# Kernel optimization log

Measured on AMD Instinct MI355X. Metric: run time of the kernel, lower is better.

Reference implementation:

```python
import jax, jax.numpy as jnp
import numpy as np
from jax.scipy.special import betainc

B, N, F_IN, D = 128, 50, 64, 64
E = N * (N - 1)          # fully-connected directed graph (no self loops)
S = N - 1                # number of ablation submodels
BN_ = B * N
EPS = 1e-5
NEG = jnp.float32(-1e9)
ALPHA = 0.05
SLOPE = 0.2              # LeakyReLU negative slope in GAT attention


def _build_graph():
    # edges grouped by target p: (c, p) for all c != p
    dst = np.repeat(np.arange(N), N - 1)
    src = np.concatenate([np.concatenate([np.arange(p), np.arange(p + 1, N)]) for p in range(N)])
    return src.astype(np.int64), dst.astype(np.int64)


def setup_inputs():
    key = jax.random.key(0)
    k = jax.random.split(key, 16)
    src, dst = _build_graph()
    edge_index = jnp.asarray(np.stack([src, dst]))
    offs = np.repeat(np.arange(B) * N, E)
    # batched edge list (get_batch_edge_index) + self loops appended (GraphLayer add_self_loops)
    src_b = jnp.asarray(np.concatenate([np.tile(src, B) + offs, np.arange(BN_)]))
    dst_b = jnp.asarray(np.concatenate([np.tile(dst, B) + offs, np.arange(BN_)]))
    # submodel s (s>=1) removes, for each target p, its (s-1)-th incoming neighbor (edge order)
    masks = np.ones((S + 1, E), dtype=bool)
    rem = np.empty((S, N), dtype=np.int64)
    for s in range(S):
        for p in range(N):
            e = p * (N - 1) + s
            masks[s + 1, e] = False
            rem[s, p] = e
    g = lambda kk, sh, sc: jax.random.normal(kk, sh, jnp.float32) * sc
    return dict(
        data=g(k[0], (B, N, F_IN), 1.0),
        labels=g(k[1], (B, N), 1.0),
        edge_index=edge_index,
        src_b=src_b, dst_b=dst_b,
        submodel_masks=jnp.asarray(masks),
        removed_edge_id=jnp.asarray(rem),
        emb=g(k[2], (N, D), 0.2),
        W_lin=g(k[3], (F_IN, D), F_IN ** -0.5),
        att_i=g(k[4], (D,), D ** -0.5), att_j=g(k[5], (D,), D ** -0.5),
        att_em_i=g(k[6], (D,), D ** -0.5), att_em_j=g(k[7], (D,), D ** -0.5),
        gat_bias=jnp.zeros((D,), jnp.float32),
        bn1_g=jnp.ones((D,), jnp.float32), bn1_b=jnp.zeros((D,), jnp.float32),
        bn1_rm=jnp.zeros((D,), jnp.float32), bn1_rv=jnp.ones((D,), jnp.float32),
        bn2_g=jnp.ones((D,), jnp.float32), bn2_b=jnp.zeros((D,), jnp.float32),
        bn2_rm=jnp.zeros((D,), jnp.float32), bn2_rv=jnp.ones((D,), jnp.float32),
        out_w=g(k[8], (D, 1), D ** -0.5), out_b=jnp.zeros((1,), jnp.float32),
    )


def reference(data, labels, edge_index, src_b, dst_b, submodel_masks, removed_edge_id,
              emb, W_lin, att_i, att_j, att_em_i, att_em_j, gat_bias,
              bn1_g, bn1_b, bn1_rm, bn1_rv, bn2_g, bn2_b, bn2_rm, bn2_rv, out_w, out_b):
    x_flat = data.reshape(BN_, F_IN)
    emb_nodes = jnp.tile(emb, (B, 1))            # all_embeddings = embedding.repeat(batch,1)

    def gnn(mask_E, train):
        # GDN-style GraphLayer: lin -> per-edge attn on (x||emb) keys -> segment softmax over dst
        emask = jnp.concatenate([jnp.tile(mask_E, B), jnp.ones(BN_, bool)])  # self loops kept
        h = x_flat @ W_lin                                  # [BN_, D]
        s_i = h @ att_i + emb_nodes @ att_em_i              # per-node dst score (key_i . att_i_cat)
        s_j = h @ att_j + emb_nodes @ att_em_j              # per-node src score
        logits = jax.nn.leaky_relu(s_i[dst_b] + s_j[src_b], SLOPE)
        logits = jnp.where(emask, logits, NEG)
        m = jax.ops.segment_max(logits, dst_b, num_segments=BN_)
        p = jnp.where(emask, jnp.exp(logits - m[dst_b]), 0.0)
        denom = jax.ops.segment_sum(p, dst_b, num_segments=BN_)
        alpha = p / denom[dst_b]
        out = jax.ops.segment_sum(alpha[:, None] * h[src_b], dst_b, num_segments=BN_) + gat_bias
        if train:
            mu, var = out.mean(0), out.var(0)               # BatchNorm1d training stats
        else:
            mu, var = bn1_rm, bn1_rv                        # eval mode (causal-edge search)
        return jax.nn.relu((out - mu) / jnp.sqrt(var + EPS) * bn1_g + bn1_b)

    def head(gcn, train):
        x3 = gcn.reshape(B, N, D) * emb[None]               # mul by node embedding
        if train:
            mu, var = x3.mean((0, 1)), x3.var((0, 1))       # BN over (B, N) per channel D
        else:
            mu, var = bn2_rm, bn2_rv
        xn = jax.nn.relu((x3 - mu) / jnp.sqrt(var + EPS) * bn2_g + bn2_b)
        return (xn @ out_w + out_b)[..., 0]                 # OutLayer (layer_num=1) -> [B,N]

    # --- causal ANOVA pruning: S+1 submodel forwards in eval mode (torch.no_grad) ---
    def body(_, mask_E):
        return None, head(gnn(mask_E, False), False)
    _, preds = jax.lax.scan(body, None, submodel_masks)     # [S+1, B, N]
    R = labels[None] - preds
    a, b = R[1:], R[0]                                      # ablated / full-graph residuals
    ma, mb = a.mean(1), b.mean(0)                           # [S,N], [N]
    grand = 0.5 * (ma + mb)
    ssb = B * ((ma - grand) ** 2 + (mb - grand) ** 2)       # between-group SS (df1=1)
    ssw = ((a - ma[:, None, :]) ** 2).sum(1) + ((b - mb) ** 2).sum(0)
    df2 = jnp.float32(2 * B - 2)
    fstat = ssb / (ssw / df2)
    pval = betainc(df2 / 2, 0.5, df2 / (df2 + fstat))       # sf of F(1, 2B-2) == f_oneway p
    prune = (pval > ALPHA).reshape(-1)                      # [S*N] == [E]
    keep = jnp.ones(E, bool).at[removed_edge_id.reshape(-1)].set(~prune)
    keep = jax.lax.stop_gradient(keep)

    # --- final forward on causally-learned graph (training-mode BN, dropout = identity) ---
    return head(gnn(keep, True), True)                      # [B, N]
```

## Files before the change

kernel.cpp:

```cpp
#include <hip/hip_runtime.h>
#include <math.h>

#define B_   128
#define N_   50
#define FIN  64
#define D_   64
#define BN   6400
#define EPSF 1e-5f
#define FCRIT 3.8783305f

__device__ __forceinline__ float wsum(float v){
#pragma unroll
  for(int o=32;o>0;o>>=1) v += __shfl_xor(v,o);
  return v;
}
__device__ __forceinline__ float wmax(float v){
#pragma unroll
  for(int o=32;o>0;o>>=1) v = fmaxf(v,__shfl_xor(v,o));
  return v;
}
__device__ __forceinline__ float leaky(float x){ return x >= 0.f ? x : 0.2f*x; }

__global__ __launch_bounds__(256) void k1_lin(
    const float* __restrict__ x, const float* __restrict__ W,
    const float* __restrict__ emb,
    const float* __restrict__ att_i, const float* __restrict__ att_j,
    const float* __restrict__ att_em_i, const float* __restrict__ att_em_j,
    const float* __restrict__ bn1_g, const float* __restrict__ bn1_b,
    const float* __restrict__ bn1_rm, const float* __restrict__ bn1_rv,
    const float* __restrict__ bn2_g, const float* __restrict__ bn2_b,
    const float* __restrict__ bn2_rm, const float* __restrict__ bn2_rv,
    const float* __restrict__ gat_bias, const float* __restrict__ out_w,
    float* __restrict__ h, float* __restrict__ s_i, float* __restrict__ s_j,
    float2* __restrict__ acc, float* __restrict__ statz ,
    float4* __restrict__ hc4, float* __restrict__ hci2g){
  __shared__ float wl[FIN*D_];
  __shared__ float xl[8*FIN];
  int tid = threadIdx.x;
  const float4* W4 = (const float4*)W;
  float4* wl4 = (float4*)wl;
  for(int i=tid;i<FIN*D_/4;i+=256) wl4[i] = W4[i];
  int r0 = blockIdx.x*8;
  { const float4* x4 = (const float4*)(x + (size_t)r0*FIN);
    float4* xl4 = (float4*)xl;
    for(int i=tid;i<8*FIN/4;i+=256) xl4[i] = x4[i]; }
  __syncthreads();
  int w = tid>>6, d = tid&63;
  float acc0 = 0.f, acc1 = 0.f;
#pragma unroll
  for(int k=0;k<FIN;k++){
    float wv = wl[k*D_+d];
    acc0 = fmaf(xl[(w*2+0)*FIN+k], wv, acc0);
    acc1 = fmaf(xl[(w*2+1)*FIN+k], wv, acc1);
  }
  float ai = att_i[d], aj = att_j[d], aei = att_em_i[d], aej = att_em_j[d];
#pragma unroll
  for(int j=0;j<2;j++){
    int r = r0 + w*2 + j;
    float a_ = j ? acc1 : acc0;
    h[(size_t)r*D_+d] = a_;
    int n = r % N_;
    float e = emb[n*D_+d];
    float si = wsum(a_*ai + e*aei);
    float sj = wsum(a_*aj + e*aej);
    if(d==0){ s_i[r]=si; s_j[r]=sj; }
  }
  if(blockIdx.x==0){
    for(int i=tid;i<N_*N_;i+=256) acc[i] = make_float2(0.f,0.f);
    for(int i=tid;i<2048;i+=256)  statz[i] = 0.f;
    if(tid < 64){
      float i1g = bn1_g[tid]/sqrtf(bn1_rv[tid]+EPSF);
      float i2g = bn2_g[tid]/sqrtf(bn2_rv[tid]+EPSF);
      float C1 = i1g*gat_bias[tid] + bn1_b[tid] - bn1_rm[tid]*i1g;
      float C2 = bn2_b[tid] - bn2_rm[tid]*i2g;
      hc4[tid] = make_float4(i1g, C1, C2, out_w[tid]);
      hci2g[tid] = i2g;
    }
  }
}

__global__ __launch_bounds__(512) void k2_preds(
    const float* __restrict__ h, const float* __restrict__ s_i,
    const float* __restrict__ s_j, const float* __restrict__ labels,
    const float* __restrict__ emb, const float* __restrict__ out_b,
    const float4* __restrict__ hc4, const float* __restrict__ hci2g,
    float2* __restrict__ acc){
  __shared__ float hT[64*53];
  __shared__ float el[8*64];
  __shared__ float2 wc[8*64];
  int b = blockIdx.y, tid = threadIdx.x;
  const float* hb = h + (size_t)b*N_*D_;
  for(int i=tid;i<N_*D_;i+=512) hT[(i&63)*53 + (i>>6)] = hb[i];
  __syncthreads();
  int w = tid>>6, lane = tid&63;
  int p = blockIdx.x*8 + w;
  if(p >= N_) return;
  float sip = s_i[b*N_+p];
  float L = -3.0e38f;
  if(lane < N_) L = leaky(sip + s_j[b*N_+lane]);
  float M = wmax(L);
  float e = (lane < N_) ? expf(L - M) : 0.f;
  float Dden = wsum(e);
  el[w*64+lane] = e;
  float S = 0.f;
  const float* hTd = &hT[lane*53];
  const float* elw = &el[w*64];
#pragma unroll 10
  for(int q=0;q<N_;q++) S = fmaf(elw[q], hTd[q], S);
  wc[w*64+lane] = make_float2(S, emb[p*D_+lane]*hci2g[lane]);
  float er = 0.f; int r = 0;
  if(lane >= 1 && lane < N_){
    int s = lane-1; r = s + (s>=p ? 1 : 0); er = el[w*64+r];
  }
  float beta = 1.f/(Dden - er);
  float alpha = er*beta;
  float acc_ = out_b[0];
  const float2* wcw = &wc[w*64];
#pragma unroll 8
  for(int d=0;d<64;d++){
    float4 hc = hc4[d];
    float2 se = wcw[d];
    float hrd = hT[d*53 + r];
    float o  = fmaf(-alpha, hrd, se.x*beta);
    float g  = fmaxf(fmaf(hc.x, o, hc.y), 0.f);
    float xn = fmaxf(fmaf(g, se.y, hc.z), 0.f);
    acc_ = fmaf(xn, hc.w, acc_);
  }
  if(lane < N_){
    float resid = labels[b*N_+p] - acc_;
    atomicAdd(&acc[p*N_+lane].x, resid);
    atomicAdd(&acc[p*N_+lane].y, resid*resid);
  }
}

__global__ __launch_bounds__(512) void k4a_out(
    const float* __restrict__ h, const float* __restrict__ s_i,
    const float* __restrict__ s_j, const float2* __restrict__ acc,
    const float* __restrict__ gat_bias,
    float* __restrict__ out_raw, float* __restrict__ stats1){
  __shared__ float hT[64*53];
  __shared__ float al[8*64];
  __shared__ int   keepL[8*64];
  __shared__ float2 red[8][64];
  int b = blockIdx.y, tid = threadIdx.x;
  const float* hb = h + (size_t)b*N_*D_;
  for(int i=tid;i<N_*D_;i+=512) hT[(i&63)*53 + (i>>6)] = hb[i];
  __syncthreads();
  int w = tid>>6, lane = tid&63;
  int p = blockIdx.x*8 + w;
  bool act = (p < N_);
  float o = 0.f;
  if(act){
    int kb = 1;
    if(lane < N_-1){
      float2 A2 = acc[p*N_ + lane + 1];
      float2 B2 = acc[p*N_];
      float ma = A2.x*(1.f/B_), mb = B2.x*(1.f/B_);
      float ssw = (A2.y - (float)B_*ma*ma) + (B2.y - (float)B_*mb*mb);
      float dmb = ma - mb;
      float f = (64.f*dmb*dmb) / (ssw*(1.f/254.f));
      kb = (f < FCRIT) ? 0 : 1;
    }
    keepL[w*64+lane] = kb;
    float sip = s_i[b*N_+p];
    float L = -3.0e38f; bool allowed = false;
    if(lane < N_){
      float Lr = leaky(sip + s_j[b*N_+lane]);
      if(lane == p) allowed = true;
      else { int idx = (lane < p) ? lane : lane-1; allowed = keepL[w*64+idx] != 0; }
      L = allowed ? Lr : -1.0e9f;
    }
    float M = wmax(L);
    float e = allowed ? expf(L - M) : 0.f;
    float Dn = wsum(e);
    al[w*64+lane] = e;
    float invD = 1.f/Dn;
    float s = 0.f;
    const float* hTd = &hT[lane*53];
    const float* alw = &al[w*64];
#pragma unroll 10
    for(int q=0;q<N_;q++) s = fmaf(alw[q], hTd[q], s);
    o = s*invD + gat_bias[lane];
    out_raw[((size_t)b*N_+p)*D_ + lane] = o;
  }
  red[w][lane] = act ? make_float2(o, o*o) : make_float2(0.f, 0.f);
  __syncthreads();
  if(w==0){
    float s1=0.f, s2=0.f;
#pragma unroll
    for(int k=0;k<8;k++){ float2 v = red[k][lane]; s1+=v.x; s2+=v.y; }
    int slot = b & 7;
    atomicAdd(&stats1[slot*128 + lane],      s1);
    atomicAdd(&stats1[slot*128 + 64 + lane], s2);
  }
}

__global__ __launch_bounds__(256) void k4b_stats(
    const float* __restrict__ out_raw, const float* __restrict__ emb,
    const float* __restrict__ bn1_g, const float* __restrict__ bn1_b,
    const float* __restrict__ stats1, float* __restrict__ stats2){
  __shared__ float2 red[4][64];
  int tid = threadIdx.x, w = tid>>6, lane = tid&63;
  float t1=0.f, t2=0.f;
#pragma unroll
  for(int k=0;k<8;k++){ t1 += stats1[k*128+lane]; t2 += stats1[k*128+64+lane]; }
  float mu1  = t1*(1.f/BN);
  float var1 = t2*(1.f/BN) - mu1*mu1;
  float A = bn1_g[lane]/sqrtf(var1+EPSF);
  float C = bn1_b[lane] - mu1*A;
  int r0 = blockIdx.x*64;
  float s1=0.f, s2=0.f;
  for(int i=w;i<64;i+=4){
    int r = r0+i;
    float o = out_raw[(size_t)r*D_ + lane];
    float g = fmaxf(fmaf(A,o,C), 0.f);
    float x3 = g*emb[(r%N_)*D_ + lane];
    s1 += x3; s2 = fmaf(x3,x3,s2);
  }
  red[w][lane] = make_float2(s1,s2);
  __syncthreads();
  if(w==0){
    float2 a=red[0][lane], b=red[1][lane], c=red[2][lane], d=red[3][lane];
    int slot = blockIdx.x & 7;
    atomicAdd(&stats2[slot*128 + lane],      a.x+b.x+c.x+d.x);
    atomicAdd(&stats2[slot*128 + 64 + lane], a.y+b.y+c.y+d.y);
  }
}

__global__ __launch_bounds__(256) void k4c_final(
    const float* __restrict__ out_raw, const float* __restrict__ emb,
    const float* __restrict__ bn1_g, const float* __restrict__ bn1_b,
    const float* __restrict__ bn2_g, const float* __restrict__ bn2_b,
    const float* __restrict__ out_w, const float* __restrict__ out_b,
    const float* __restrict__ stats1, const float* __restrict__ stats2,
    float* __restrict__ outp){
  int tid = threadIdx.x, w = tid>>6, lane = tid&63;
  float t1=0.f, t2=0.f, t3=0.f, t4=0.f;
#pragma unroll
  for(int k=0;k<8;k++){
    t1 += stats1[k*128+lane]; t2 += stats1[k*128+64+lane];
    t3 += stats2[k*128+lane]; t4 += stats2[k*128+64+lane];
  }
  float mu1  = t1*(1.f/BN), var1 = t2*(1.f/BN) - mu1*mu1;
  float mu2  = t3*(1.f/BN), var2 = t4*(1.f/BN) - mu2*mu2;
  float A1 = bn1_g[lane]/sqrtf(var1+EPSF);
  float C1 = bn1_b[lane] - mu1*A1;
  float A2 = bn2_g[lane]/sqrtf(var2+EPSF);
  float C2 = bn2_b[lane] - mu2*A2;
  float ow = out_w[lane], ob = out_b[0];
#pragma unroll
  for(int j=0;j<4;j++){
    int r = blockIdx.x*16 + w*4 + j;
    float o = out_raw[(size_t)r*D_ + lane];
    float g = fmaxf(fmaf(A1,o,C1), 0.f);
    float x3 = g*emb[(r%N_)*D_ + lane];
    float xn = fmaxf(fmaf(A2,x3,C2), 0.f);
    float pr = wsum(xn*ow);
    if(lane==0) outp[r] = pr + ob;
  }
}

extern "C" void kernel_launch(void* const* d_in, const int* in_sizes, int n_in,
                              void* d_out, int out_size, void* d_ws, size_t ws_size,
                              hipStream_t stream){
  (void)in_sizes; (void)n_in; (void)out_size; (void)ws_size;
  const float* data     = (const float*)d_in[0];
  const float* labels   = (const float*)d_in[1];
  const float* emb      = (const float*)d_in[7];
  const float* W_lin    = (const float*)d_in[8];
  const float* att_i    = (const float*)d_in[9];
  const float* att_j    = (const float*)d_in[10];
  const float* att_em_i = (const float*)d_in[11];
  const float* att_em_j = (const float*)d_in[12];
  const float* gat_bias = (const float*)d_in[13];
  const float* bn1_g    = (const float*)d_in[14];
  const float* bn1_b    = (const float*)d_in[15];
  const float* bn1_rm   = (const float*)d_in[16];
  const float* bn1_rv   = (const float*)d_in[17];
  const float* bn2_g    = (const float*)d_in[18];
  const float* bn2_b    = (const float*)d_in[19];
  const float* bn2_rm   = (const float*)d_in[20];
  const float* bn2_rv   = (const float*)d_in[21];
  const float* out_w    = (const float*)d_in[22];
  const float* out_b    = (const float*)d_in[23];

  float*  ws      = (float*)d_ws;
  float*  h       = ws;
  float*  s_i     = ws + 409600;
  float*  s_j     = ws + 416000;
  float*  out_raw = ws + 422400;
  float2* acc     = (float2*)(ws + 832000);
  float*  stats1  = ws + 837000;
  float*  stats2  = ws + 838024;
  float4* hc4     = (float4*)(ws + 839048);
  float*  hci2g   = ws + 839304;
  float*  outp    = (float*)d_out;

  hipLaunchKernelGGL(k1_lin, dim3(BN/8), dim3(256), 0, stream,
                     data, W_lin, emb, att_i, att_j, att_em_i, att_em_j,
                     bn1_g, bn1_b, bn1_rm, bn1_rv, bn2_g, bn2_b, bn2_rm, bn2_rv,
                     gat_bias, out_w, h, s_i, s_j, acc, stats1, hc4, hci2g);
  hipLaunchKernelGGL(k2_preds, dim3(7, B_), dim3(512), 0, stream,
                     h, s_i, s_j, labels, emb, out_b, hc4, hci2g, acc);
  hipLaunchKernelGGL(k4a_out, dim3(7, B_), dim3(512), 0, stream,
                     h, s_i, s_j, acc, gat_bias, out_raw, stats1);
  hipLaunchKernelGGL(k4b_stats, dim3(BN/64), dim3(256), 0, stream,
                     out_raw, emb, bn1_g, bn1_b, stats1, stats2);
  hipLaunchKernelGGL(k4c_final, dim3(BN/16), dim3(256), 0, stream,
                     out_raw, emb, bn1_g, bn1_b, bn2_g, bn2_b, out_w, out_b,
                     stats1, stats2, outp);
}
```

Baseline: 142.9 us.

## Fuse all stages into one cooperative kernel with grid syncs and LDS-resident h

Replaces the five kernel launches with one cooperative kernel of 256 blocks, two per batch element, each covering 25 target nodes. The linear projection, attention scores, submodel residual accumulation, pruned-graph GAT output and both batch-norm stat passes are separated by grid.sync. Each block keeps its batch's h, scores and outputs in shared memory, so the global round trips for h, s_i/s_j and out_raw go away along with the launch gaps. In exchange it adds four grid-wide barriers, and each block recomputes the full 50-row projection for its batch, doubling that work.

```diff
diff --git a/kernel.cpp b/kernel.cpp
--- a/kernel.cpp
+++ b/kernel.cpp
@@ -1,9 +1,11 @@
 #include <hip/hip_runtime.h>
+#include <hip/hip_cooperative_groups.h>
 #include <math.h>
+
+namespace cg = cooperative_groups;
 
 #define B_   128
 #define N_   50
-#define FIN  64
 #define D_   64
 #define BN   6400
 #define EPSF 1e-5f
@@ -21,54 +23,44 @@
 }
 __device__ __forceinline__ float leaky(float x){ return x >= 0.f ? x : 0.2f*x; }
 
-__global__ __launch_bounds__(256) void k1_lin(
-    const float* __restrict__ x, const float* __restrict__ W,
-    const float* __restrict__ emb,
+__global__ __launch_bounds__(512) void fused(
+    const float* __restrict__ x, const float* __restrict__ labels,
+    const float* __restrict__ emb, const float* __restrict__ W,
     const float* __restrict__ att_i, const float* __restrict__ att_j,
     const float* __restrict__ att_em_i, const float* __restrict__ att_em_j,
+    const float* __restrict__ gat_bias,
     const float* __restrict__ bn1_g, const float* __restrict__ bn1_b,
     const float* __restrict__ bn1_rm, const float* __restrict__ bn1_rv,
     const float* __restrict__ bn2_g, const float* __restrict__ bn2_b,
     const float* __restrict__ bn2_rm, const float* __restrict__ bn2_rv,
-    const float* __restrict__ gat_bias, const float* __restrict__ out_w,
-    float* __restrict__ h, float* __restrict__ s_i, float* __restrict__ s_j,
-    float2* __restrict__ acc, float* __restrict__ statz ,
-    float4* __restrict__ hc4, float* __restrict__ hci2g){
-  __shared__ float wl[FIN*D_];
-  __shared__ float xl[8*FIN];
-  int tid = threadIdx.x;
-  const float4* W4 = (const float4*)W;
-  float4* wl4 = (float4*)wl;
-  for(int i=tid;i<FIN*D_/4;i+=256) wl4[i] = W4[i];
-  int r0 = blockIdx.x*8;
-  { const float4* x4 = (const float4*)(x + (size_t)r0*FIN);
-    float4* xl4 = (float4*)xl;
-    for(int i=tid;i<8*FIN/4;i+=256) xl4[i] = x4[i]; }
-  __syncthreads();
-  int w = tid>>6, d = tid&63;
-  float acc0 = 0.f, acc1 = 0.f;
-#pragma unroll
-  for(int k=0;k<FIN;k++){
-    float wv = wl[k*D_+d];
-    acc0 = fmaf(xl[(w*2+0)*FIN+k], wv, acc0);
-    acc1 = fmaf(xl[(w*2+1)*FIN+k], wv, acc1);
-  }
-  float ai = att_i[d], aj = att_j[d], aei = att_em_i[d], aej = att_em_j[d];
-#pragma unroll
-  for(int j=0;j<2;j++){
-    int r = r0 + w*2 + j;
-    float a_ = j ? acc1 : acc0;
-    h[(size_t)r*D_+d] = a_;
-    int n = r % N_;
-    float e = emb[n*D_+d];
-    float si = wsum(a_*ai + e*aei);
-    float sj = wsum(a_*aj + e*aej);
-    if(d==0){ s_i[r]=si; s_j[r]=sj; }
-  }
-  if(blockIdx.x==0){
-    for(int i=tid;i<N_*N_;i+=256) acc[i] = make_float2(0.f,0.f);
-    for(int i=tid;i<2048;i+=256)  statz[i] = 0.f;
-    if(tid < 64){
+    const float* __restrict__ out_w, const float* __restrict__ out_b,
+    float2* __restrict__ acc, float* __restrict__ stats1,
+    float* __restrict__ stats2, float4* __restrict__ hc4,
+    float* __restrict__ hci2g, float* __restrict__ outp){
+  __shared__ float wl[64*64];
+  __shared__ float xl[50*65];
+  __shared__ float hT[64*53];
+  __shared__ float sl_i[64], sl_j[64];
+  __shared__ float el[8*64];
+  __shared__ float2 wc[8*64];
+  __shared__ int   keepL[8*64];
+  __shared__ float outL[25*64];
+  __shared__ float2 red[8][64];
+
+  cg::grid_group grid = cg::this_grid();
+  int tid = threadIdx.x, w = tid>>6, lane = tid&63;
+  int blk = blockIdx.x;
+  int b = blk>>1, p0 = (blk&1)*25;
+
+  { const float4* W4 = (const float4*)W;
+    float4* wl4 = (float4*)wl;
+    for(int i=tid;i<1024;i+=512) wl4[i] = W4[i]; }
+  { const float* xb = x + (size_t)b*N_*64;
+    for(int i=tid;i<3200;i+=512) xl[(i>>6)*65 + (i&63)] = xb[i]; }
+  if(blk==0){
+    for(int i=tid;i<N_*N_;i+=512) acc[i] = make_float2(0.f,0.f);
+    for(int i=tid;i<1024;i+=512){ stats1[i]=0.f; stats2[i]=0.f; }
+    if(tid<64){
       float i1g = bn1_g[tid]/sqrtf(bn1_rv[tid]+EPSF);
       float i2g = bn2_g[tid]/sqrtf(bn2_rv[tid]+EPSF);
       float C1 = i1g*gat_bias[tid] + bn1_b[tid] - bn1_rm[tid]*i1g;
@@ -77,80 +69,84 @@
       hci2g[tid] = i2g;
     }
   }
-}
-
-__global__ __launch_bounds__(512) void k2_preds(
-    const float* __restrict__ h, const float* __restrict__ s_i,
-    const float* __restrict__ s_j, const float* __restrict__ labels,
-    const float* __restrict__ emb, const float* __restrict__ out_b,
-    const float4* __restrict__ hc4, const float* __restrict__ hci2g,
-    float2* __restrict__ acc){
-  __shared__ float hT[64*53];
-  __shared__ float el[8*64];
-  __shared__ float2 wc[8*64];
-  int b = blockIdx.y, tid = threadIdx.x;
-  const float* hb = h + (size_t)b*N_*D_;
-  for(int i=tid;i<N_*D_;i+=512) hT[(i&63)*53 + (i>>6)] = hb[i];
-  __syncthreads();
-  int w = tid>>6, lane = tid&63;
-  int p = blockIdx.x*8 + w;
-  if(p >= N_) return;
-  float sip = s_i[b*N_+p];
-  float L = -3.0e38f;
-  if(lane < N_) L = leaky(sip + s_j[b*N_+lane]);
-  float M = wmax(L);
-  float e = (lane < N_) ? expf(L - M) : 0.f;
-  float Dden = wsum(e);
-  el[w*64+lane] = e;
-  float S = 0.f;
-  const float* hTd = &hT[lane*53];
-  const float* elw = &el[w*64];
+  __syncthreads();
+
+#pragma unroll
+  for(int it=0; it<2; ++it){
+    int idx4 = tid + it*512;
+    if(idx4 < 800){
+      int q = idx4 >> 4, d4 = idx4 & 15;
+      const float4* wrow = (const float4*)wl;
+      float4 a = make_float4(0.f,0.f,0.f,0.f);
+#pragma unroll
+      for(int k=0;k<64;k++){
+        float xv = xl[q*65+k];
+        float4 wv = wrow[k*16+d4];
+        a.x=fmaf(xv,wv.x,a.x); a.y=fmaf(xv,wv.y,a.y);
+        a.z=fmaf(xv,wv.z,a.z); a.w=fmaf(xv,wv.w,a.w);
+      }
+      int d0 = d4*4;
+      hT[(d0  )*53+q]=a.x; hT[(d0+1)*53+q]=a.y;
+      hT[(d0+2)*53+q]=a.z; hT[(d0+3)*53+q]=a.w;
+    }
+  }
+  __syncthreads();
+
+  for(int q=w; q<N_; q+=8){
+    float hv = hT[lane*53+q];
+    float ev = emb[q*64+lane];
+    float si = wsum(fmaf(hv, att_i[lane], ev*att_em_i[lane]));
+    float sj = wsum(fmaf(hv, att_j[lane], ev*att_em_j[lane]));
+    if(lane==0){ sl_i[q]=si; sl_j[q]=sj; }
+  }
+  __syncthreads();
+  __threadfence();
+  grid.sync();
+
+  float ob = out_b[0];
+  for(int pi=w; pi<25; pi+=8){
+    int p = p0 + pi;
+    float sip = sl_i[p];
+    float L = -3.0e38f;
+    if(lane<N_) L = leaky(sip + sl_j[lane]);
+    float M = wmax(L);
+    float e = (lane<N_) ? expf(L-M) : 0.f;
+    float Dden = wsum(e);
+    el[w*64+lane] = e;
+    float S = 0.f;
+    const float* hTd = &hT[lane*53];
+    const float* elw = &el[w*64];
 #pragma unroll 10
-  for(int q=0;q<N_;q++) S = fmaf(elw[q], hTd[q], S);
-  wc[w*64+lane] = make_float2(S, emb[p*D_+lane]*hci2g[lane]);
-  float er = 0.f; int r = 0;
-  if(lane >= 1 && lane < N_){
-    int s = lane-1; r = s + (s>=p ? 1 : 0); er = el[w*64+r];
-  }
-  float beta = 1.f/(Dden - er);
-  float alpha = er*beta;
-  float acc_ = out_b[0];
-  const float2* wcw = &wc[w*64];
+    for(int q=0;q<N_;q++) S = fmaf(elw[q], hTd[q], S);
+    wc[w*64+lane] = make_float2(S, emb[p*64+lane]*hci2g[lane]);
+    float er = 0.f; int r = 0;
+    if(lane>=1 && lane<N_){ int s=lane-1; r = s + (s>=p?1:0); er = el[w*64+r]; }
+    float beta  = 1.f/(Dden - er);
+    float alpha = er*beta;
+    float a_ = ob;
+    const float2* wcw = &wc[w*64];
 #pragma unroll 8
-  for(int d=0;d<64;d++){
-    float4 hc = hc4[d];
-    float2 se = wcw[d];
-    float hrd = hT[d*53 + r];
-    float o  = fmaf(-alpha, hrd, se.x*beta);
-    float g  = fmaxf(fmaf(hc.x, o, hc.y), 0.f);
-    float xn = fmaxf(fmaf(g, se.y, hc.z), 0.f);
-    acc_ = fmaf(xn, hc.w, acc_);
-  }
-  if(lane < N_){
-    float resid = labels[b*N_+p] - acc_;
-    atomicAdd(&acc[p*N_+lane].x, resid);
-    atomicAdd(&acc[p*N_+lane].y, resid*resid);
-  }
-}
-
-__global__ __launch_bounds__(512) void k4a_out(
-    const float* __restrict__ h, const float* __restrict__ s_i,
-    const float* __restrict__ s_j, const float2* __restrict__ acc,
-    const float* __restrict__ gat_bias,
-    float* __restrict__ out_raw, float* __restrict__ stats1){
-  __shared__ float hT[64*53];
-  __shared__ float al[8*64];
-  __shared__ int   keepL[8*64];
-  __shared__ float2 red[8][64];
-  int b = blockIdx.y, tid = threadIdx.x;
-  const float* hb = h + (size_t)b*N_*D_;
-  for(int i=tid;i<N_*D_;i+=512) hT[(i&63)*53 + (i>>6)] = hb[i];
-  __syncthreads();
-  int w = tid>>6, lane = tid&63;
-  int p = blockIdx.x*8 + w;
-  bool act = (p < N_);
-  float o = 0.f;
-  if(act){
+    for(int d=0;d<64;d++){
+      float4 hc = hc4[d];
+      float2 se = wcw[d];
+      float hrd = hT[d*53 + r];
+      float o  = fmaf(-alpha, hrd, se.x*beta);
+      float g  = fmaxf(fmaf(hc.x, o, hc.y), 0.f);
+      float xn = fmaxf(fmaf(g, se.y, hc.z), 0.f);
+      a_ = fmaf(xn, hc.w, a_);
+    }
+    if(lane<N_){
+      float resid = labels[b*N_+p] - a_;
+      atomicAdd(&acc[p*N_+lane].x, resid);
+      atomicAdd(&acc[p*N_+lane].y, resid*resid);
+    }
+  }
+  __threadfence();
+  grid.sync();
+
+  float s1=0.f, s2=0.f;
+  for(int pi=w; pi<25; pi+=8){
+    int p = p0 + pi;
     int kb = 1;
     if(lane < N_-1){
       float2 A2 = acc[p*N_ + lane + 1];
@@ -162,101 +158,83 @@
       kb = (f < FCRIT) ? 0 : 1;
     }
     keepL[w*64+lane] = kb;
-    float sip = s_i[b*N_+p];
+    float sip = sl_i[p];
     float L = -3.0e38f; bool allowed = false;
-    if(lane < N_){
-      float Lr = leaky(sip + s_j[b*N_+lane]);
-      if(lane == p) allowed = true;
-      else { int idx = (lane < p) ? lane : lane-1; allowed = keepL[w*64+idx] != 0; }
+    if(lane<N_){
+      float Lr = leaky(sip + sl_j[lane]);
+      if(lane==p) allowed = true;
+      else { int idx = (lane<p)?lane:lane-1; allowed = keepL[w*64+idx]!=0; }
       L = allowed ? Lr : -1.0e9f;
     }
     float M = wmax(L);
-    float e = allowed ? expf(L - M) : 0.f;
+    float e = allowed ? expf(L-M) : 0.f;
     float Dn = wsum(e);
-    al[w*64+lane] = e;
+    el[w*64+lane] = e;
     float invD = 1.f/Dn;
     float s = 0.f;
     const float* hTd = &hT[lane*53];
-    const float* alw = &al[w*64];
+    const float* elw = &el[w*64];
 #pragma unroll 10
-    for(int q=0;q<N_;q++) s = fmaf(alw[q], hTd[q], s);
-    o = s*invD + gat_bias[lane];
-    out_raw[((size_t)b*N_+p)*D_ + lane] = o;
-  }
-  red[w][lane] = act ? make_float2(o, o*o) : make_float2(0.f, 0.f);
+    for(int q=0;q<N_;q++) s = fmaf(elw[q], hTd[q], s);
+    float o = fmaf(s, invD, gat_bias[lane]);
+    outL[pi*64+lane] = o;
+    s1 += o; s2 = fmaf(o,o,s2);
+  }
+  red[w][lane] = make_float2(s1,s2);
   __syncthreads();
   if(w==0){
-    float s1=0.f, s2=0.f;
-#pragma unroll
-    for(int k=0;k<8;k++){ float2 v = red[k][lane]; s1+=v.x; s2+=v.y; }
-    int slot = b & 7;
-    atomicAdd(&stats1[slot*128 + lane],      s1);
-    atomicAdd(&stats1[slot*128 + 64 + lane], s2);
-  }
-}
-
-__global__ __launch_bounds__(256) void k4b_stats(
-    const float* __restrict__ out_raw, const float* __restrict__ emb,
-    const float* __restrict__ bn1_g, const float* __restrict__ bn1_b,
-    const float* __restrict__ stats1, float* __restrict__ stats2){
-  __shared__ float2 red[4][64];
-  int tid = threadIdx.x, w = tid>>6, lane = tid&63;
+    float a1=0.f, a2=0.f;
+#pragma unroll
+    for(int k=0;k<8;k++){ float2 v = red[k][lane]; a1+=v.x; a2+=v.y; }
+    int slot = blk & 7;
+    atomicAdd(&stats1[slot*128 + lane],      a1);
+    atomicAdd(&stats1[slot*128 + 64 + lane], a2);
+  }
+  __threadfence();
+  grid.sync();
+
   float t1=0.f, t2=0.f;
 #pragma unroll
   for(int k=0;k<8;k++){ t1 += stats1[k*128+lane]; t2 += stats1[k*128+64+lane]; }
-  float mu1  = t1*(1.f/BN);
-  float var1 = t2*(1.f/BN) - mu1*mu1;
-  float A = bn1_g[lane]/sqrtf(var1+EPSF);
-  float C = bn1_b[lane] - mu1*A;
-  int r0 = blockIdx.x*64;
-  float s1=0.f, s2=0.f;
-  for(int i=w;i<64;i+=4){
-    int r = r0+i;
-    float o = out_raw[(size_t)r*D_ + lane];
-    float g = fmaxf(fmaf(A,o,C), 0.f);
-    float x3 = g*emb[(r%N_)*D_ + lane];
-    s1 += x3; s2 = fmaf(x3,x3,s2);
-  }
-  red[w][lane] = make_float2(s1,s2);
-  __syncthreads();
-  if(w==0){
-    float2 a=red[0][lane], b=red[1][lane], c=red[2][lane], d=red[3][lane];
-    int slot = blockIdx.x & 7;
-    atomicAdd(&stats2[slot*128 + lane],      a.x+b.x+c.x+d.x);
-    atomicAdd(&stats2[slot*128 + 64 + lane], a.y+b.y+c.y+d.y);
-  }
-}
-
-__global__ __launch_bounds__(256) void k4c_final(
-    const float* __restrict__ out_raw, const float* __restrict__ emb,
-    const float* __restrict__ bn1_g, const float* __restrict__ bn1_b,
-    const float* __restrict__ bn2_g, const float* __restrict__ bn2_b,
-    const float* __restrict__ out_w, const float* __restrict__ out_b,
-    const float* __restrict__ stats1, const float* __restrict__ stats2,
-    float* __restrict__ outp){
-  int tid = threadIdx.x, w = tid>>6, lane = tid&63;
-  float t1=0.f, t2=0.f, t3=0.f, t4=0.f;
-#pragma unroll
-  for(int k=0;k<8;k++){
-    t1 += stats1[k*128+lane]; t2 += stats1[k*128+64+lane];
-    t3 += stats2[k*128+lane]; t4 += stats2[k*128+64+lane];
-  }
   float mu1  = t1*(1.f/BN), var1 = t2*(1.f/BN) - mu1*mu1;
-  float mu2  = t3*(1.f/BN), var2 = t4*(1.f/BN) - mu2*mu2;
   float A1 = bn1_g[lane]/sqrtf(var1+EPSF);
   float C1 = bn1_b[lane] - mu1*A1;
+  s1=0.f; s2=0.f;
+  for(int pi=w; pi<25; pi+=8){
+    int p = p0 + pi;
+    float o  = outL[pi*64+lane];
+    float g  = fmaxf(fmaf(A1,o,C1), 0.f);
+    float x3 = g*emb[p*64+lane];
+    s1 += x3; s2 = fmaf(x3,x3,s2);
+  }
+  red[w][lane] = make_float2(s1,s2);
+  __syncthreads();
+  if(w==0){
+    float a1=0.f, a2=0.f;
+#pragma unroll
+    for(int k=0;k<8;k++){ float2 v = red[k][lane]; a1+=v.x; a2+=v.y; }
+    int slot = blk & 7;
+    atomicAdd(&stats2[slot*128 + lane],      a1);
+    atomicAdd(&stats2[slot*128 + 64 + lane], a2);
+  }
+  __threadfence();
+  grid.sync();
+
+  float t3=0.f, t4=0.f;
+#pragma unroll
+  for(int k=0;k<8;k++){ t3 += stats2[k*128+lane]; t4 += stats2[k*128+64+lane]; }
+  float mu2  = t3*(1.f/BN), var2 = t4*(1.f/BN) - mu2*mu2;
   float A2 = bn2_g[lane]/sqrtf(var2+EPSF);
   float C2 = bn2_b[lane] - mu2*A2;
-  float ow = out_w[lane], ob = out_b[0];
-#pragma unroll
-  for(int j=0;j<4;j++){
-    int r = blockIdx.x*16 + w*4 + j;
-    float o = out_raw[(size_t)r*D_ + lane];
-    float g = fmaxf(fmaf(A1,o,C1), 0.f);
-    float x3 = g*emb[(r%N_)*D_ + lane];
+  float ow = out_w[lane];
+  for(int pi=w; pi<25; pi+=8){
+    int p = p0 + pi;
+    float o  = outL[pi*64+lane];
+    float g  = fmaxf(fmaf(A1,o,C1), 0.f);
+    float x3 = g*emb[p*64+lane];
     float xn = fmaxf(fmaf(A2,x3,C2), 0.f);
     float pr = wsum(xn*ow);
-    if(lane==0) outp[r] = pr + ob;
+    if(lane==0) outp[b*N_+p] = pr + ob;
   }
 }
 
@@ -284,29 +262,24 @@
   const float* out_w    = (const float*)d_in[22];
   const float* out_b    = (const float*)d_in[23];
 
-  float*  ws      = (float*)d_ws;
-  float*  h       = ws;
-  float*  s_i     = ws + 409600;
-  float*  s_j     = ws + 416000;
-  float*  out_raw = ws + 422400;
-  float2* acc     = (float2*)(ws + 832000);
-  float*  stats1  = ws + 837000;
-  float*  stats2  = ws + 838024;
-  float4* hc4     = (float4*)(ws + 839048);
-  float*  hci2g   = ws + 839304;
-  float*  outp    = (float*)d_out;
-
-  hipLaunchKernelGGL(k1_lin, dim3(BN/8), dim3(256), 0, stream,
-                     data, W_lin, emb, att_i, att_j, att_em_i, att_em_j,
-                     bn1_g, bn1_b, bn1_rm, bn1_rv, bn2_g, bn2_b, bn2_rm, bn2_rv,
-                     gat_bias, out_w, h, s_i, s_j, acc, stats1, hc4, hci2g);
-  hipLaunchKernelGGL(k2_preds, dim3(7, B_), dim3(512), 0, stream,
-                     h, s_i, s_j, labels, emb, out_b, hc4, hci2g, acc);
-  hipLaunchKernelGGL(k4a_out, dim3(7, B_), dim3(512), 0, stream,
-                     h, s_i, s_j, acc, gat_bias, out_raw, stats1);
-  hipLaunchKernelGGL(k4b_stats, dim3(BN/64), dim3(256), 0, stream,
-                     out_raw, emb, bn1_g, bn1_b, stats1, stats2);
-  hipLaunchKernelGGL(k4c_final, dim3(BN/16), dim3(256), 0, stream,
-                     out_raw, emb, bn1_g, bn1_b, bn2_g, bn2_b, out_w, out_b,
-                     stats1, stats2, outp);
-}
+  float*  ws     = (float*)d_ws;
+  float2* acc    = (float2*)ws;
+  float*  stats1 = ws + 5120;
+  float*  stats2 = ws + 6144;
+  float4* hc4    = (float4*)(ws + 7168);
+  float*  hci2g  = ws + 7424;
+  float*  outp   = (float*)d_out;
+
+  void* args[] = {
+    (void*)&data, (void*)&labels, (void*)&emb, (void*)&W_lin,
+    (void*)&att_i, (void*)&att_j, (void*)&att_em_i, (void*)&att_em_j,
+    (void*)&gat_bias,
+    (void*)&bn1_g, (void*)&bn1_b, (void*)&bn1_rm, (void*)&bn1_rv,
+    (void*)&bn2_g, (void*)&bn2_b, (void*)&bn2_rm, (void*)&bn2_rv,
+    (void*)&out_w, (void*)&out_b,
+    (void*)&acc, (void*)&stats1, (void*)&stats2, (void*)&hc4,
+    (void*)&hci2g, (void*)&outp
+  };
+  hipLaunchCooperativeKernel((const void*)fused, dim3(2*B_), dim3(512),
+                             args, 0, stream);
+}
```

New measurement: 402.6 us. +181.7%, slower.

## Fuse linear projection and attention scores into submodel prediction kernel per batch

Applied to the files above, without the earlier changes.

Merges the linear-projection/attention-score kernel into the ablation prediction kernel. Each block now recomputes h for one batch (50x64) in shared memory and derives s_i/s_j locally, and only blockIdx.x==0 writes them back for later kernels. Zeroing of the accumulators moves to a hipMemsetAsync. This removes a launch and a global round trip of h. In exchange the grid shrinks from 7xB to 2xB blocks, lowering parallelism, and the matmul is done twice per batch.

```diff
diff --git a/kernel.cpp b/kernel.cpp
--- a/kernel.cpp
+++ b/kernel.cpp
@@ -21,9 +21,9 @@
 }
 __device__ __forceinline__ float leaky(float x){ return x >= 0.f ? x : 0.2f*x; }
 
-__global__ __launch_bounds__(256) void k1_lin(
-    const float* __restrict__ x, const float* __restrict__ W,
-    const float* __restrict__ emb,
+__global__ __launch_bounds__(512) void k2m(
+    const float* __restrict__ x, const float* __restrict__ labels,
+    const float* __restrict__ emb, const float* __restrict__ W,
     const float* __restrict__ att_i, const float* __restrict__ att_j,
     const float* __restrict__ att_em_i, const float* __restrict__ att_em_j,
     const float* __restrict__ bn1_g, const float* __restrict__ bn1_b,
@@ -31,105 +31,109 @@
     const float* __restrict__ bn2_g, const float* __restrict__ bn2_b,
     const float* __restrict__ bn2_rm, const float* __restrict__ bn2_rv,
     const float* __restrict__ gat_bias, const float* __restrict__ out_w,
+    const float* __restrict__ out_b,
     float* __restrict__ h, float* __restrict__ s_i, float* __restrict__ s_j,
-    float2* __restrict__ acc, float* __restrict__ statz ,
-    float4* __restrict__ hc4, float* __restrict__ hci2g){
-  __shared__ float wl[FIN*D_];
-  __shared__ float xl[8*FIN];
-  int tid = threadIdx.x;
-  const float4* W4 = (const float4*)W;
-  float4* wl4 = (float4*)wl;
-  for(int i=tid;i<FIN*D_/4;i+=256) wl4[i] = W4[i];
-  int r0 = blockIdx.x*8;
-  { const float4* x4 = (const float4*)(x + (size_t)r0*FIN);
-    float4* xl4 = (float4*)xl;
-    for(int i=tid;i<8*FIN/4;i+=256) xl4[i] = x4[i]; }
-  __syncthreads();
-  int w = tid>>6, d = tid&63;
-  float acc0 = 0.f, acc1 = 0.f;
-#pragma unroll
-  for(int k=0;k<FIN;k++){
-    float wv = wl[k*D_+d];
-    acc0 = fmaf(xl[(w*2+0)*FIN+k], wv, acc0);
-    acc1 = fmaf(xl[(w*2+1)*FIN+k], wv, acc1);
-  }
-  float ai = att_i[d], aj = att_j[d], aei = att_em_i[d], aej = att_em_j[d];
-#pragma unroll
-  for(int j=0;j<2;j++){
-    int r = r0 + w*2 + j;
-    float a_ = j ? acc1 : acc0;
-    h[(size_t)r*D_+d] = a_;
-    int n = r % N_;
-    float e = emb[n*D_+d];
-    float si = wsum(a_*ai + e*aei);
-    float sj = wsum(a_*aj + e*aej);
-    if(d==0){ s_i[r]=si; s_j[r]=sj; }
-  }
-  if(blockIdx.x==0){
-    for(int i=tid;i<N_*N_;i+=256) acc[i] = make_float2(0.f,0.f);
-    for(int i=tid;i<2048;i+=256)  statz[i] = 0.f;
-    if(tid < 64){
-      float i1g = bn1_g[tid]/sqrtf(bn1_rv[tid]+EPSF);
-      float i2g = bn2_g[tid]/sqrtf(bn2_rv[tid]+EPSF);
-      float C1 = i1g*gat_bias[tid] + bn1_b[tid] - bn1_rm[tid]*i1g;
-      float C2 = bn2_b[tid] - bn2_rm[tid]*i2g;
-      hc4[tid] = make_float4(i1g, C1, C2, out_w[tid]);
-      hci2g[tid] = i2g;
-    }
-  }
-}
-
-__global__ __launch_bounds__(512) void k2_preds(
-    const float* __restrict__ h, const float* __restrict__ s_i,
-    const float* __restrict__ s_j, const float* __restrict__ labels,
-    const float* __restrict__ emb, const float* __restrict__ out_b,
-    const float4* __restrict__ hc4, const float* __restrict__ hci2g,
     float2* __restrict__ acc){
+  __shared__ float wl[64*64];
+  __shared__ float xl[50*65];
   __shared__ float hT[64*53];
+  __shared__ float sl_i[64], sl_j[64];
   __shared__ float el[8*64];
   __shared__ float2 wc[8*64];
-  int b = blockIdx.y, tid = threadIdx.x;
-  const float* hb = h + (size_t)b*N_*D_;
-  for(int i=tid;i<N_*D_;i+=512) hT[(i&63)*53 + (i>>6)] = hb[i];
-  __syncthreads();
-  int w = tid>>6, lane = tid&63;
-  int p = blockIdx.x*8 + w;
-  if(p >= N_) return;
-  float sip = s_i[b*N_+p];
-  float L = -3.0e38f;
-  if(lane < N_) L = leaky(sip + s_j[b*N_+lane]);
-  float M = wmax(L);
-  float e = (lane < N_) ? expf(L - M) : 0.f;
-  float Dden = wsum(e);
-  el[w*64+lane] = e;
-  float S = 0.f;
-  const float* hTd = &hT[lane*53];
-  const float* elw = &el[w*64];
+  __shared__ float4 hcl[64];
+  __shared__ float  hil[64];
+  int tid = threadIdx.x, w = tid>>6, lane = tid&63;
+  int b = blockIdx.y, p0 = blockIdx.x*25;
+
+  { const float4* W4 = (const float4*)W;
+    float4* wl4 = (float4*)wl;
+    for(int i=tid;i<1024;i+=512) wl4[i] = W4[i]; }
+  { const float* xb = x + (size_t)b*N_*64;
+    for(int i=tid;i<3200;i+=512) xl[(i>>6)*65 + (i&63)] = xb[i]; }
+  if(tid<64){
+    float i1g = bn1_g[tid]/sqrtf(bn1_rv[tid]+EPSF);
+    float i2g = bn2_g[tid]/sqrtf(bn2_rv[tid]+EPSF);
+    float C1 = i1g*gat_bias[tid] + bn1_b[tid] - bn1_rm[tid]*i1g;
+    float C2 = bn2_b[tid] - bn2_rm[tid]*i2g;
+    hcl[tid] = make_float4(i1g, C1, C2, out_w[tid]);
+    hil[tid] = i2g;
+  }
+  __syncthreads();
+
+#pragma unroll
+  for(int it=0; it<2; ++it){
+    int idx4 = tid + it*512;
+    if(idx4 < 800){
+      int q = idx4 >> 4, d4 = idx4 & 15;
+      const float4* wrow = (const float4*)wl;
+      float4 a = make_float4(0.f,0.f,0.f,0.f);
+#pragma unroll
+      for(int k=0;k<64;k++){
+        float xv = xl[q*65+k];
+        float4 wv = wrow[k*16+d4];
+        a.x=fmaf(xv,wv.x,a.x); a.y=fmaf(xv,wv.y,a.y);
+        a.z=fmaf(xv,wv.z,a.z); a.w=fmaf(xv,wv.w,a.w);
+      }
+      int d0 = d4*4;
+      hT[(d0  )*53+q]=a.x; hT[(d0+1)*53+q]=a.y;
+      hT[(d0+2)*53+q]=a.z; hT[(d0+3)*53+q]=a.w;
+      if(blockIdx.x==0){
+        float4* hg = (float4*)(h + (size_t)b*N_*64);
+        hg[q*16+d4] = a;
+      }
+    }
+  }
+  __syncthreads();
+
+  for(int q=w; q<N_; q+=8){
+    float hv = hT[lane*53+q];
+    float ev = emb[q*64+lane];
+    float si = wsum(fmaf(hv, att_i[lane], ev*att_em_i[lane]));
+    float sj = wsum(fmaf(hv, att_j[lane], ev*att_em_j[lane]));
+    if(lane==0){
+      sl_i[q]=si; sl_j[q]=sj;
+      if(blockIdx.x==0){ s_i[b*N_+q]=si; s_j[b*N_+q]=sj; }
+    }
+  }
+  __syncthreads();
+
+  float ob = out_b[0];
+  for(int pi=w; pi<25; pi+=8){
+    int p = p0 + pi;
+    float sip = sl_i[p];
+    float L = -3.0e38f;
+    if(lane<N_) L = leaky(sip + sl_j[lane]);
+    float M = wmax(L);
+    float e = (lane<N_) ? expf(L-M) : 0.f;
+    float Dden = wsum(e);
+    el[w*64+lane] = e;
+    float S = 0.f;
+    const float* hTd = &hT[lane*53];
+    const float* elw = &el[w*64];
 #pragma unroll 10
-  for(int q=0;q<N_;q++) S = fmaf(elw[q], hTd[q], S);
-  wc[w*64+lane] = make_float2(S, emb[p*D_+lane]*hci2g[lane]);
-  float er = 0.f; int r = 0;
-  if(lane >= 1 && lane < N_){
-    int s = lane-1; r = s + (s>=p ? 1 : 0); er = el[w*64+r];
-  }
-  float beta = 1.f/(Dden - er);
-  float alpha = er*beta;
-  float acc_ = out_b[0];
-  const float2* wcw = &wc[w*64];
+    for(int q=0;q<N_;q++) S = fmaf(elw[q], hTd[q], S);
+    wc[w*64+lane] = make_float2(S, emb[p*64+lane]*hil[lane]);
+    float er = 0.f; int r = 0;
+    if(lane>=1 && lane<N_){ int s=lane-1; r = s + (s>=p?1:0); er = el[w*64+r]; }
+    float beta  = 1.f/(Dden - er);
+    float alpha = er*beta;
+    float a_ = ob;
+    const float2* wcw = &wc[w*64];
 #pragma unroll 8
-  for(int d=0;d<64;d++){
-    float4 hc = hc4[d];
-    float2 se = wcw[d];
-    float hrd = hT[d*53 + r];
-    float o  = fmaf(-alpha, hrd, se.x*beta);
-    float g  = fmaxf(fmaf(hc.x, o, hc.y), 0.f);
-    float xn = fmaxf(fmaf(g, se.y, hc.z), 0.f);
-    acc_ = fmaf(xn, hc.w, acc_);
-  }
-  if(lane < N_){
-    float resid = labels[b*N_+p] - acc_;
-    atomicAdd(&acc[p*N_+lane].x, resid);
-    atomicAdd(&acc[p*N_+lane].y, resid*resid);
+    for(int d=0;d<64;d++){
+      float4 hc = hcl[d];
+      float2 se = wcw[d];
+      float hrd = hT[d*53 + r];
+      float o  = fmaf(-alpha, hrd, se.x*beta);
+      float g  = fmaxf(fmaf(hc.x, o, hc.y), 0.f);
+      float xn = fmaxf(fmaf(g, se.y, hc.z), 0.f);
+      a_ = fmaf(xn, hc.w, a_);
+    }
+    if(lane<N_){
+      float resid = labels[b*N_+p] - a_;
+      atomicAdd(&acc[p*N_+lane].x, resid);
+      atomicAdd(&acc[p*N_+lane].y, resid*resid);
+    }
   }
 }
 
@@ -180,18 +184,18 @@
     const float* alw = &al[w*64];
 #pragma unroll 10
     for(int q=0;q<N_;q++) s = fmaf(alw[q], hTd[q], s);
-    o = s*invD + gat_bias[lane];
+    o = fmaf(s, invD, gat_bias[lane]);
     out_raw[((size_t)b*N_+p)*D_ + lane] = o;
   }
   red[w][lane] = act ? make_float2(o, o*o) : make_float2(0.f, 0.f);
   __syncthreads();
   if(w==0){
-    float s1=0.f, s2=0.f;
-#pragma unroll
-    for(int k=0;k<8;k++){ float2 v = red[k][lane]; s1+=v.x; s2+=v.y; }
+    float a1=0.f, a2=0.f;
+#pragma unroll
+    for(int k=0;k<8;k++){ float2 v = red[k][lane]; a1+=v.x; a2+=v.y; }
     int slot = b & 7;
-    atomicAdd(&stats1[slot*128 + lane],      s1);
-    atomicAdd(&stats1[slot*128 + 64 + lane], s2);
+    atomicAdd(&stats1[slot*128 + lane],      a1);
+    atomicAdd(&stats1[slot*128 + 64 + lane], a2);
   }
 }
 
@@ -292,16 +296,14 @@
   float2* acc     = (float2*)(ws + 832000);
   float*  stats1  = ws + 837000;
   float*  stats2  = ws + 838024;
-  float4* hc4     = (float4*)(ws + 839048);
-  float*  hci2g   = ws + 839304;
   float*  outp    = (float*)d_out;
 
-  hipLaunchKernelGGL(k1_lin, dim3(BN/8), dim3(256), 0, stream,
-                     data, W_lin, emb, att_i, att_j, att_em_i, att_em_j,
+  hipMemsetAsync((void*)(ws + 832000), 0, (839048 - 832000)*sizeof(float), stream);
+
+  hipLaunchKernelGGL(k2m, dim3(2, B_), dim3(512), 0, stream,
+                     data, labels, emb, W_lin, att_i, att_j, att_em_i, att_em_j,
                      bn1_g, bn1_b, bn1_rm, bn1_rv, bn2_g, bn2_b, bn2_rm, bn2_rv,
-                     gat_bias, out_w, h, s_i, s_j, acc, stats1, hc4, hci2g);
-  hipLaunchKernelGGL(k2_preds, dim3(7, B_), dim3(512), 0, stream,
-                     h, s_i, s_j, labels, emb, out_b, hc4, hci2g, acc);
+                     gat_bias, out_w, out_b, h, s_i, s_j, acc);
   hipLaunchKernelGGL(k4a_out, dim3(7, B_), dim3(512), 0, stream,
                      h, s_i, s_j, acc, gat_bias, out_raw, stats1);
   hipLaunchKernelGGL(k4b_stats, dim3(BN/64), dim3(256), 0, stream,
```

Result: slower. 158.3 us (+10.8%).
